# Optimization experiments

Hardware: AMD Instinct MI355X
Metric: run time of the kernel (lower is better)

## Reference

```python
import jax, jax.numpy as jnp
import numpy as np
import math

GROUPS = 32
EPS = 1e-5
NUM_HEADS = 8


def group_norm(x, gamma, beta):
    # x: [B, C, T]
    B, C, T = x.shape
    xg = x.reshape(B, GROUPS, C // GROUPS, T)
    mean = xg.mean(axis=(2, 3), keepdims=True)
    var = xg.var(axis=(2, 3), keepdims=True)
    xn = (xg - mean) * jax.lax.rsqrt(var + EPS)
    return xn.reshape(B, C, T) * gamma[None, :, None] + beta[None, :, None]


def qkv_attention(qkv, num_heads):
    # qkv: [B, 3C, T]
    B, C3, T = qkv.shape
    split = C3 // (3 * num_heads)  # head dim
    q, k, v = jnp.split(qkv, 3, axis=1)
    scale = 1.0 / math.sqrt(math.sqrt(split))
    q = (q * scale).reshape(B * num_heads, split, T)
    k = (k * scale).reshape(B * num_heads, split, T)
    v = v.reshape(B * num_heads, split, T)
    w = jnp.einsum('bct,bcs->bts', q, k)
    w = jax.nn.softmax(w.astype(jnp.float32), axis=-1).astype(w.dtype)
    out = jnp.einsum('bts,bcs->bct', w, v)
    return out.reshape(B, -1, T)


def setup_inputs() -> dict:
    key = jax.random.key(0)
    ks = jax.random.split(key, 6)
    B, C, H, W = 16, 512, 32, 32
    x = jax.random.normal(ks[0], (B, C, H, W), dtype=jnp.float32)
    gamma = jnp.ones((C,), jnp.float32)
    beta = jnp.zeros((C,), jnp.float32)
    w_qkv = jax.random.normal(ks[1], (3 * C, C), jnp.float32) * (1.0 / math.sqrt(C))
    b_qkv = jax.random.normal(ks[2], (3 * C,), jnp.float32) * 0.01
    # proj is zero-initialized in the module; use small random weights so the
    # full op chain (proj + residual) is numerically exercised.
    w_proj = jax.random.normal(ks[3], (C, C), jnp.float32) * (1.0 / math.sqrt(C))
    b_proj = jax.random.normal(ks[4], (C,), jnp.float32) * 0.01
    return {"x": x, "gamma": gamma, "beta": beta, "w_qkv": w_qkv,
            "b_qkv": b_qkv, "w_proj": w_proj, "b_proj": b_proj}


def reference(x, gamma, beta, w_qkv, b_qkv, w_proj, b_proj):
    b, c = x.shape[0], x.shape[1]
    spatial = x.shape[2:]
    xf = x.reshape(b, c, -1)                     # [B, C, T]
    xn = group_norm(xf, gamma, beta)
    qkv = jnp.einsum('oc,bct->bot', w_qkv, xn) + b_qkv[None, :, None]
    h = qkv_attention(qkv, NUM_HEADS)
    h = jnp.einsum('oc,bct->bot', w_proj, h) + b_proj[None, :, None]
    # NOTE: residual uses the normalized x (x is reassigned before norm in torch code)
    return (xn + h).reshape(b, c, *spatial)
```

## Files before the change

### kernel.cpp

```cpp
#include <hip/hip_runtime.h>

typedef __attribute__((ext_vector_type(8))) short s16x8;
typedef __attribute__((ext_vector_type(8))) unsigned short u16x8;
typedef __attribute__((ext_vector_type(4))) float f32x4;
typedef __attribute__((ext_vector_type(16))) float f32x16;

#define DEV static __device__ __forceinline__

DEV unsigned short f2bf(float f){
  union { float f; unsigned u; } v; v.f = f;
  unsigned u = v.u;
  return (unsigned short)((u + 0x7FFFu + ((u >> 16) & 1u)) >> 16);
}

DEV unsigned cvt_pk(float lo, float hi){
  unsigned r;
  asm("v_cvt_pk_bf16_f32 %0, %1, %2" : "=v"(r) : "v"(lo), "v"(hi));
  return r;
}

DEV void pl32_swap(unsigned &d, unsigned &s){
  asm("v_permlane32_swap_b32 %0, %1" : "+v"(d), "+v"(s));
}

DEV void gload16(const void* g, void* l){
  __builtin_amdgcn_global_load_lds((const __attribute__((address_space(1))) void*)g,
                                   (__attribute__((address_space(3))) void*)l, 16, 0, 0);
}

__global__ __launch_bounds__(256) void k_gncvt(const float* __restrict__ x,
    const float* __restrict__ gamma, const float* __restrict__ beta,
    float* __restrict__ stats, unsigned short* __restrict__ xt,
    const float* __restrict__ w_qkv, const float* __restrict__ w_proj,
    unsigned short* __restrict__ w_bf){
  __shared__ unsigned short lt[1024 * 16];
  __shared__ float red[8];
  __shared__ float sh_ms[2];
  const int bid = blockIdx.x;
  const int tid = threadIdx.x;

  if (bid >= 512){
    int i = (bid - 512) * 256 + tid;
    const float4* src = (i < 196608) ? (const float4*)w_qkv + i
                                     : (const float4*)w_proj + (i - 196608);
    float4 v = *src;
    unsigned long long p = (unsigned long long)f2bf(v.x)
                         | ((unsigned long long)f2bf(v.y) << 16)
                         | ((unsigned long long)f2bf(v.z) << 32)
                         | ((unsigned long long)f2bf(v.w) << 48);
    *(unsigned long long*)(w_bf + (size_t)i * 4) = p;
    return;
  }

  const int b = bid >> 5, g = bid & 31;
  const float* base = x + ((size_t)(b * 512 + g * 16)) * 1024;

  float4 vv[16];
  float s = 0.f, ss = 0.f;
  #pragma unroll
  for (int i = 0; i < 16; ++i){
    vv[i] = *(const float4*)(base + i * 1024 + tid * 4);
    s  += vv[i].x + vv[i].y + vv[i].z + vv[i].w;
    ss += vv[i].x * vv[i].x + vv[i].y * vv[i].y + vv[i].z * vv[i].z + vv[i].w * vv[i].w;
  }
  #pragma unroll
  for (int d = 1; d < 64; d <<= 1){ s += __shfl_xor(s, d); ss += __shfl_xor(ss, d); }
  if ((tid & 63) == 0){ red[tid >> 6] = s; red[4 + (tid >> 6)] = ss; }
  __syncthreads();
  if (tid == 0){
    float ts  = red[0] + red[1] + red[2] + red[3];
    float tss = red[4] + red[5] + red[6] + red[7];
    float mean = ts * (1.f / 16384.f);
    float var  = tss * (1.f / 16384.f) - mean * mean;
    float rstd = rsqrtf(var + 1e-5f);
    sh_ms[0] = mean; sh_ms[1] = rstd;
    stats[(size_t)bid * 2] = mean;
    stats[(size_t)bid * 2 + 1] = rstd;
  }
  __syncthreads();
  const float mean = sh_ms[0], rstd = sh_ms[1];

  unsigned short vals[4][16];
  #pragma unroll
  for (int i = 0; i < 16; ++i){
    float gsc = gamma[g * 16 + i] * rstd;
    float bof = beta[g * 16 + i] - mean * gsc;
    vals[0][i] = f2bf(vv[i].x * gsc + bof);
    vals[1][i] = f2bf(vv[i].y * gsc + bof);
    vals[2][i] = f2bf(vv[i].z * gsc + bof);
    vals[3][i] = f2bf(vv[i].w * gsc + bof);
  }
  #pragma unroll
  for (int k2 = 0; k2 < 4; ++k2){
    u16x8 lo, hi;
    #pragma unroll
    for (int e = 0; e < 8; ++e){ lo[e] = vals[k2][e]; hi[e] = vals[k2][8 + e]; }
    int t = tid * 4 + k2;
    *(u16x8*)&lt[t * 16]     = lo;
    *(u16x8*)&lt[t * 16 + 8] = hi;
  }
  __syncthreads();
  unsigned short* dst = xt + ((size_t)b * 1024) * 512 + g * 16;
  #pragma unroll
  for (int j = 0; j < 8; ++j){
    int idx = j * 256 + tid;
    int t = idx >> 1, half = idx & 1;
    u16x8 v = *(const u16x8*)&lt[t * 16 + half * 8];
    *(u16x8*)(dst + (size_t)t * 512 + half * 8) = v;
  }
}

DEV void gemm_mainloop(const unsigned short* __restrict__ pA,
                       const unsigned short* __restrict__ pB,
                       unsigned short* As, unsigned short* Bs,
                       f32x4 (&acc)[4][4], int tid){
  const int lane = tid & 63, wv = tid >> 6;
  const int wr = wv >> 1, wc = wv & 1;
  const int ro = lane & 15;
  for (int k0 = 0; k0 < 512; k0 += 64){
    #pragma unroll
    for (int it = 0; it < 4; ++it){
      int chunk = it * 256 + tid;
      int r = chunk >> 3, sb = chunk & 7;
      size_t goff = (size_t)r * 512 + k0 + ((sb ^ (r & 7)) << 3);
      gload16(pA + goff, As + (size_t)(it * 256 + wv * 64) * 8);
      gload16(pB + goff, Bs + (size_t)(it * 256 + wv * 64) * 8);
    }
    __syncthreads();
    #pragma unroll
    for (int kk = 0; kk < 2; ++kk){
      s16x8 a[4], bb[4];
      int ko = kk * 64 + ((lane >> 4) << 4);
      #pragma unroll
      for (int i2 = 0; i2 < 4; ++i2){
        int ra = wr * 64 + i2 * 16 + ro;
        a[i2]  = *(const s16x8*)((const char*)As + ra * 128 + (ko ^ ((ra & 7) << 4)));
        int rb = wc * 64 + i2 * 16 + ro;
        bb[i2] = *(const s16x8*)((const char*)Bs + rb * 128 + (ko ^ ((rb & 7) << 4)));
      }
      __builtin_amdgcn_s_setprio(1);
      #pragma unroll
      for (int i2 = 0; i2 < 4; ++i2)
        #pragma unroll
        for (int j2 = 0; j2 < 4; ++j2)
          acc[i2][j2] = __builtin_amdgcn_mfma_f32_16x16x32_bf16(a[i2], bb[j2], acc[i2][j2], 0, 0, 0);
      __builtin_amdgcn_s_setprio(0);
    }
    __syncthreads();
  }
}

__global__ __launch_bounds__(256) void k_qkv(const unsigned short* __restrict__ W,
    const unsigned short* __restrict__ Xt, const float* __restrict__ bias,
    unsigned short* __restrict__ qkt, unsigned short* __restrict__ vbuf){
  __shared__ unsigned short As[128 * 64], Bs[128 * 64];
  const int bid = blockIdx.x;
  const int nt = bid & 7; const int tmp = bid >> 3;
  const int mt = tmp % 12, b = tmp / 12;
  const int tid = threadIdx.x;
  const unsigned short* Wt = W + (size_t)mt * 128 * 512;
  const unsigned short* Xb = Xt + ((size_t)(b * 1024) + nt * 128) * 512;
  f32x4 acc[4][4];
  #pragma unroll
  for (int i = 0; i < 4; ++i)
    #pragma unroll
    for (int j = 0; j < 4; ++j) acc[i][j] = f32x4{0.f, 0.f, 0.f, 0.f};
  const bool isv = (mt >= 8);
  if (isv) gemm_mainloop(Wt, Xb, As, Bs, acc, tid);
  else     gemm_mainloop(Xb, Wt, As, Bs, acc, tid);
  const int lane = tid & 63, wv = tid >> 6, wr = wv >> 1, wc = wv & 1;
  const int col = lane & 15, rq = (lane >> 4) << 2;
  if (isv){
    #pragma unroll
    for (int i = 0; i < 4; ++i){
      #pragma unroll
      for (int jj = 0; jj < 4; ++jj){
        int og = mt * 128 + wr * 64 + i * 16 + rq + jj;
        float bv = bias[og];
        unsigned short* drow = vbuf + ((size_t)(b * 512) + (og - 1024)) * 1024 + nt * 128 + wc * 64;
        #pragma unroll
        for (int j = 0; j < 4; ++j)
          drow[j * 16 + col] = f2bf(acc[i][j][jj] + bv);
      }
    }
  } else {
    #pragma unroll
    for (int i = 0; i < 4; ++i){
      #pragma unroll
      for (int jj = 0; jj < 4; ++jj){
        int tg = nt * 128 + wr * 64 + i * 16 + rq + jj;
        unsigned short* drow = qkt + ((size_t)(b * 1024) + tg) * 1024 + mt * 128 + wc * 64;
        #pragma unroll
        for (int j = 0; j < 4; ++j){
          int og = mt * 128 + wc * 64 + j * 16 + col;
          drow[j * 16 + col] = f2bf(acc[i][j][jj] + bias[og]);
        }
      }
    }
  }
}

__global__ __launch_bounds__(256, 4) void k_attn(const unsigned short* __restrict__ qkt,
    const unsigned short* __restrict__ vbuf, unsigned short* __restrict__ ht){
  __shared__ __align__(16) unsigned short smem[16384];

  const int bid = blockIdx.x;
  const int xcd = bid & 7, slot = bid >> 3;
  const int qt = slot & 7;
  const int b = slot >> 3, h = xcd;
  const int tid = threadIdx.x, lane = tid & 63, wv = tid >> 6;
  const int l31 = lane & 31, hi = lane >> 5;
  const int wq0 = qt * 128 + wv * 32;
  const float CSC = 0.125f * 1.44269504f;
  const float M0 = 8.f;

  s16x8 qf[4];
  {
    const unsigned short* qrow = qkt + ((size_t)(b * 1024) + wq0 + l31) * 1024 + h * 64 + hi * 8;
    #pragma unroll
    for (int kk = 0; kk < 4; ++kk)
      qf[kk] = *(const s16x8*)(qrow + kk * 16);
  }

  f32x16 o_acc[2];
  #pragma unroll
  for (int mi = 0; mi < 2; ++mi)
    #pragma unroll
    for (int e = 0; e < 16; ++e) o_acc[mi][e] = 0.f;
  float l_run = 0.f;

  const int r0 = tid >> 3;
  const int so = ((tid & 7) ^ (r0 & 7)) << 3;
  const unsigned short* pK = qkt + (size_t)(b * 1024) * 1024 + 512 + h * 64
                           + (size_t)r0 * 1024 + so;
  const unsigned short* pV = vbuf + ((size_t)(b * 512) + h * 64) * 1024
                           + (size_t)r0 * 1024 + so;
  const size_t IT1 = (size_t)32 * 1024;

  #define STAGE(bsel) do {                                                   \
    unsigned short* Kd = smem + (bsel) * 8192;                               \
    unsigned short* Vd = Kd + 4096;                                          \
    gload16(pK,       Kd + (size_t)(wv * 64) * 8);                           \
    gload16(pK + IT1, Kd + (size_t)(256 + wv * 64) * 8);                     \
    gload16(pV,       Vd + (size_t)(wv * 64) * 8);                           \
    gload16(pV + IT1, Vd + (size_t)(256 + wv * 64) * 8);                     \
    pK += 64 * 1024; pV += 64;                                               \
  } while (0)

  STAGE(0);
  __syncthreads();
  int cur = 0;

  for (int t = 0; t < 16; ++t){
    if (t < 15) STAGE(cur ^ 1);
    const unsigned short* Ks = smem + cur * 8192;
    const unsigned short* Vs = Ks + 4096;

    f32x16 sa[2];
    #pragma unroll
    for (int ni = 0; ni < 2; ++ni)
      #pragma unroll
      for (int e = 0; e < 16; ++e) sa[ni][e] = 0.f;
    #pragma unroll
    for (int kk = 0; kk < 4; ++kk){
      s16x8 kf[2];
      #pragma unroll
      for (int ni = 0; ni < 2; ++ni){
        int r = ni * 32 + l31;
        kf[ni] = *(const s16x8*)((const char*)Ks + r * 128 + ((kk * 32 + hi * 16) ^ ((r & 7) << 4)));
      }
      __builtin_amdgcn_s_setprio(1);
      sa[0] = __builtin_amdgcn_mfma_f32_32x32x16_bf16(kf[0], qf[kk], sa[0], 0, 0, 0);
      sa[1] = __builtin_amdgcn_mfma_f32_32x32x16_bf16(kf[1], qf[kk], sa[1], 0, 0, 0);
      __builtin_amdgcn_s_setprio(0);
    }

    float rsa = 0.f, rsb = 0.f;
    unsigned pk[2][4][2];
    #pragma unroll
    for (int ni = 0; ni < 2; ++ni)
      #pragma unroll
      for (int rr = 0; rr < 4; ++rr){
        float p0 = __builtin_amdgcn_exp2f(fmaf(sa[ni][4 * rr + 0], CSC, -M0));
        float p1 = __builtin_amdgcn_exp2f(fmaf(sa[ni][4 * rr + 1], CSC, -M0));
        float p2 = __builtin_amdgcn_exp2f(fmaf(sa[ni][4 * rr + 2], CSC, -M0));
        float p3 = __builtin_amdgcn_exp2f(fmaf(sa[ni][4 * rr + 3], CSC, -M0));
        rsa += p0 + p1;
        rsb += p2 + p3;
        pk[ni][rr][0] = cvt_pk(p0, p1);
        pk[ni][rr][1] = cvt_pk(p2, p3);
      }
    {
      union { float f; unsigned u; } ua, ub;
      ua.f = rsa + rsb; ub.u = ua.u;
      pl32_swap(ua.u, ub.u);
      l_run += ua.f + ub.f;
    }

    #pragma unroll
    for (int ks = 0; ks < 4; ++ks){
      int ni = ks >> 1, q2 = (ks & 1) * 2;
      unsigned d0 = pk[ni][q2][0],     d1 = pk[ni][q2][1];
      unsigned s0 = pk[ni][q2 + 1][0], s1 = pk[ni][q2 + 1][1];
      pl32_swap(d0, s0);
      pl32_swap(d1, s1);
      union { unsigned u[4]; s16x8 v; } pb;
      pb.u[0] = d0;
      pb.u[1] = d1;
      pb.u[2] = s0;
      pb.u[3] = s1;
      s16x8 vf[2];
      #pragma unroll
      for (int mi = 0; mi < 2; ++mi){
        int c = mi * 32 + l31;
        vf[mi] = *(const s16x8*)((const char*)Vs + c * 128 + ((ks * 32 + hi * 16) ^ ((c & 7) << 4)));
      }
      __builtin_amdgcn_s_setprio(1);
      o_acc[0] = __builtin_amdgcn_mfma_f32_32x32x16_bf16(vf[0], pb.v, o_acc[0], 0, 0, 0);
      o_acc[1] = __builtin_amdgcn_mfma_f32_32x32x16_bf16(vf[1], pb.v, o_acc[1], 0, 0, 0);
      __builtin_amdgcn_s_setprio(0);
    }

    asm volatile("s_waitcnt vmcnt(0)" ::: "memory");
    __builtin_amdgcn_sched_barrier(0);
    __syncthreads();
    cur ^= 1;
  }
  #undef STAGE

  float invl = 1.f / l_run;
  unsigned short* ow = smem + wv * 2048;
  int t = l31;
  #pragma unroll
  for (int mi = 0; mi < 2; ++mi)
    #pragma unroll
    for (int rr = 0; rr < 4; ++rr){
      int c0 = mi * 32 + 8 * rr + 4 * hi;
      unsigned d0 = cvt_pk(o_acc[mi][4 * rr + 0] * invl, o_acc[mi][4 * rr + 1] * invl);
      unsigned d1 = cvt_pk(o_acc[mi][4 * rr + 2] * invl, o_acc[mi][4 * rr + 3] * invl);
      unsigned* dst = (unsigned*)(ow + t * 64 + (c0 ^ ((t & 7) << 3)));
      dst[0] = d0; dst[1] = d1;
    }
  __syncthreads();
  unsigned short* hbase = ht + ((size_t)(b * 1024) + wq0) * 512 + h * 64;
  #pragma unroll
  for (int i = 0; i < 4; ++i){
    int id = i * 64 + lane;
    int tl = id >> 3, c8 = id & 7;
    u16x8 v = *(const u16x8*)(ow + tl * 64 + ((c8 ^ (tl & 7)) << 3));
    *(u16x8*)(hbase + (size_t)tl * 512 + c8 * 8) = v;
  }
}

__global__ __launch_bounds__(256) void k_proj(const unsigned short* __restrict__ Wp,
    const unsigned short* __restrict__ Ht, const float* __restrict__ bias,
    const float* __restrict__ x, const float* __restrict__ stats,
    const float* __restrict__ gamma, const float* __restrict__ beta,
    float* __restrict__ out){
  __shared__ unsigned short As[128 * 64], Bs[128 * 64];
  const int bid = blockIdx.x;
  const int nt = bid & 7, mt = (bid >> 3) & 3, b = bid >> 5;
  const int tid = threadIdx.x;
  f32x4 acc[4][4];
  #pragma unroll
  for (int i = 0; i < 4; ++i)
    #pragma unroll
    for (int j = 0; j < 4; ++j) acc[i][j] = f32x4{0.f, 0.f, 0.f, 0.f};
  gemm_mainloop(Wp + (size_t)mt * 128 * 512,
                Ht + ((size_t)(b * 1024) + nt * 128) * 512, As, Bs, acc, tid);
  const int lane = tid & 63, wv = tid >> 6, wr = wv >> 1, wc = wv & 1;
  const int col = lane & 15, rq = (lane >> 4) << 2;
  #pragma unroll
  for (int i = 0; i < 4; ++i){
    #pragma unroll
    for (int jj = 0; jj < 4; ++jj){
      int og = mt * 128 + wr * 64 + i * 16 + rq + jj;
      float mean = stats[(size_t)(b * 32 + (og >> 4)) * 2];
      float rstd = stats[(size_t)(b * 32 + (og >> 4)) * 2 + 1];
      float gsc = gamma[og] * rstd;
      float bof = beta[og] - mean * gsc + bias[og];
      const float* xrow = x  + ((size_t)(b * 512) + og) * 1024 + nt * 128 + wc * 64;
      float* orow      = out + ((size_t)(b * 512) + og) * 1024 + nt * 128 + wc * 64;
      #pragma unroll
      for (int j = 0; j < 4; ++j){
        float xv = xrow[j * 16 + col];
        orow[j * 16 + col] = acc[i][j][jj] + xv * gsc + bof;
      }
    }
  }
}

extern "C" void kernel_launch(void* const* d_in, const int* in_sizes, int n_in,
                              void* d_out, int out_size, void* d_ws, size_t ws_size,
                              hipStream_t stream) {
  (void)in_sizes; (void)n_in; (void)out_size; (void)ws_size;
  const float* x      = (const float*)d_in[0];
  const float* gamma  = (const float*)d_in[1];
  const float* beta   = (const float*)d_in[2];
  const float* w_qkv  = (const float*)d_in[3];
  const float* b_qkv  = (const float*)d_in[4];
  const float* w_proj = (const float*)d_in[5];
  const float* b_proj = (const float*)d_in[6];
  float* out = (float*)d_out;
  char* ws = (char*)d_ws;

  unsigned short* wq_bf = (unsigned short*)ws;
  unsigned short* wp_bf = (unsigned short*)(ws + 1572864);
  float*          stats = (float*)(ws + 2097152);
  unsigned short* Xt    = (unsigned short*)(ws + 2101248);
  unsigned short* qkt   = (unsigned short*)(ws + 18878464);
  unsigned short* vbuf  = (unsigned short*)(ws + 52432896);

  k_gncvt<<<1536, 256, 0, stream>>>(x, gamma, beta, stats, Xt, w_qkv, w_proj, wq_bf);
  k_qkv<<<1536, 256, 0, stream>>>(wq_bf, Xt, b_qkv, qkt, vbuf);
  unsigned short* Ht = Xt;
  k_attn<<<1024, 256, 0, stream>>>(qkt, vbuf, Ht);
  k_proj<<<512, 256, 0, stream>>>(wp_bf, Ht, b_proj, x, stats, gamma, beta, out);
}
```

Measured before the change: 119.5 us.

## Load attention K/V fragments directly from global memory instead of LDS staging

Drops the double-buffered LDS staging of K and V tiles in the attention kernel. Each wave now loads its MFMA operand fragments straight from global memory into registers, and the per-iteration barriers and waitcnt go away. Shared memory is halved to just what the output transpose needs. In exchange, the four waves of a block each fetch the same K/V data redundantly through the cache, and global load latency is no longer hidden by explicit prefetching.

```diff
diff --git a/kernel.cpp b/kernel.cpp
--- a/kernel.cpp
+++ b/kernel.cpp
@@ -202,7 +202,7 @@
 
 __global__ __launch_bounds__(256, 4) void k_attn(const unsigned short* __restrict__ qkt,
     const unsigned short* __restrict__ vbuf, unsigned short* __restrict__ ht){
-  __shared__ __align__(16) unsigned short smem[16384];
+  __shared__ __align__(16) unsigned short smem[8192];
 
   const int bid = blockIdx.x;
   const int xcd = bid & 7, slot = bid >> 3;
@@ -229,32 +229,18 @@
     for (int e = 0; e < 16; ++e) o_acc[mi][e] = 0.f;
   float l_run = 0.f;
 
-  const int r0 = tid >> 3;
-  const int so = ((tid & 7) ^ (r0 & 7)) << 3;
-  const unsigned short* pK = qkt + (size_t)(b * 1024) * 1024 + 512 + h * 64
-                           + (size_t)r0 * 1024 + so;
-  const unsigned short* pV = vbuf + ((size_t)(b * 512) + h * 64) * 1024
-                           + (size_t)r0 * 1024 + so;
-  const size_t IT1 = (size_t)32 * 1024;
-
-  #define STAGE(bsel) do {                                                   \
-    unsigned short* Kd = smem + (bsel) * 8192;                               \
-    unsigned short* Vd = Kd + 4096;                                          \
-    gload16(pK,       Kd + (size_t)(wv * 64) * 8);                           \
-    gload16(pK + IT1, Kd + (size_t)(256 + wv * 64) * 8);                     \
-    gload16(pV,       Vd + (size_t)(wv * 64) * 8);                           \
-    gload16(pV + IT1, Vd + (size_t)(256 + wv * 64) * 8);                     \
-    pK += 64 * 1024; pV += 64;                                               \
-  } while (0)
-
-  STAGE(0);
-  __syncthreads();
-  int cur = 0;
+  const unsigned short* pK0 = qkt + ((size_t)(b * 1024) + l31) * 1024 + 512 + h * 64 + hi * 8;
+  const unsigned short* pK1 = pK0 + (size_t)32 * 1024;
+  const unsigned short* pV0 = vbuf + ((size_t)(b * 512) + h * 64 + l31) * 1024 + hi * 8;
+  const unsigned short* pV1 = pV0 + (size_t)32 * 1024;
 
   for (int t = 0; t < 16; ++t){
-    if (t < 15) STAGE(cur ^ 1);
-    const unsigned short* Ks = smem + cur * 8192;
-    const unsigned short* Vs = Ks + 4096;
+    s16x8 kf[4][2];
+    #pragma unroll
+    for (int kk = 0; kk < 4; ++kk){
+      kf[kk][0] = *(const s16x8*)(pK0 + kk * 16);
+      kf[kk][1] = *(const s16x8*)(pK1 + kk * 16);
+    }
 
     f32x16 sa[2];
     #pragma unroll
@@ -263,15 +249,9 @@
       for (int e = 0; e < 16; ++e) sa[ni][e] = 0.f;
     #pragma unroll
     for (int kk = 0; kk < 4; ++kk){
-      s16x8 kf[2];
-      #pragma unroll
-      for (int ni = 0; ni < 2; ++ni){
-        int r = ni * 32 + l31;
-        kf[ni] = *(const s16x8*)((const char*)Ks + r * 128 + ((kk * 32 + hi * 16) ^ ((r & 7) << 4)));
-      }
       __builtin_amdgcn_s_setprio(1);
-      sa[0] = __builtin_amdgcn_mfma_f32_32x32x16_bf16(kf[0], qf[kk], sa[0], 0, 0, 0);
-      sa[1] = __builtin_amdgcn_mfma_f32_32x32x16_bf16(kf[1], qf[kk], sa[1], 0, 0, 0);
+      sa[0] = __builtin_amdgcn_mfma_f32_32x32x16_bf16(kf[kk][0], qf[kk], sa[0], 0, 0, 0);
+      sa[1] = __builtin_amdgcn_mfma_f32_32x32x16_bf16(kf[kk][1], qf[kk], sa[1], 0, 0, 0);
       __builtin_amdgcn_s_setprio(0);
     }
 
@@ -309,24 +289,17 @@
       pb.u[1] = d1;
       pb.u[2] = s0;
       pb.u[3] = s1;
-      s16x8 vf[2];
-      #pragma unroll
-      for (int mi = 0; mi < 2; ++mi){
-        int c = mi * 32 + l31;
-        vf[mi] = *(const s16x8*)((const char*)Vs + c * 128 + ((ks * 32 + hi * 16) ^ ((c & 7) << 4)));
-      }
+      s16x8 vf0 = *(const s16x8*)(pV0 + ks * 16);
+      s16x8 vf1 = *(const s16x8*)(pV1 + ks * 16);
       __builtin_amdgcn_s_setprio(1);
-      o_acc[0] = __builtin_amdgcn_mfma_f32_32x32x16_bf16(vf[0], pb.v, o_acc[0], 0, 0, 0);
-      o_acc[1] = __builtin_amdgcn_mfma_f32_32x32x16_bf16(vf[1], pb.v, o_acc[1], 0, 0, 0);
+      o_acc[0] = __builtin_amdgcn_mfma_f32_32x32x16_bf16(vf0, pb.v, o_acc[0], 0, 0, 0);
+      o_acc[1] = __builtin_amdgcn_mfma_f32_32x32x16_bf16(vf1, pb.v, o_acc[1], 0, 0, 0);
       __builtin_amdgcn_s_setprio(0);
     }
 
-    asm volatile("s_waitcnt vmcnt(0)" ::: "memory");
-    __builtin_amdgcn_sched_barrier(0);
-    __syncthreads();
-    cur ^= 1;
-  }
-  #undef STAGE
+    pK0 += (size_t)64 * 1024; pK1 += (size_t)64 * 1024;
+    pV0 += 64; pV1 += 64;
+  }
 
   float invl = 1.f / l_run;
   unsigned short* ow = smem + wv * 2048;
```

Result: slower. 190.2 us (+59.2%).

## Reuse bf16 normalized activations for residual and write attention output into qkt

Applied to the files above, without the earlier changes.

The attention output is now written in place into the Q/K buffer (row stride 1024) instead of overwriting Xt, which keeps the bf16 normalized activations alive. The projection epilogue then reads the residual from that bf16 Xt tile, staged through shared memory, instead of re-reading fp32 x and recomputing the normalization from stored stats and gamma/beta. This halves residual read traffic and drops the stats buffer, at the cost of a bf16-rounded residual and a transposed LDS staging step. Overwriting qkt assumes each attention block has finished reading its Q/K rows before it writes them.

```diff
diff --git a/kernel.cpp b/kernel.cpp
--- a/kernel.cpp
+++ b/kernel.cpp
@@ -2,6 +2,7 @@
 
 typedef __attribute__((ext_vector_type(8))) short s16x8;
 typedef __attribute__((ext_vector_type(8))) unsigned short u16x8;
+typedef __attribute__((ext_vector_type(4))) unsigned short u16x4;
 typedef __attribute__((ext_vector_type(4))) float f32x4;
 typedef __attribute__((ext_vector_type(16))) float f32x16;
 
@@ -13,6 +14,11 @@
   return (unsigned short)((u + 0x7FFFu + ((u >> 16) & 1u)) >> 16);
 }
 
+DEV float bf2f(unsigned short b){
+  union { unsigned u; float f; } v; v.u = ((unsigned)b) << 16;
+  return v.f;
+}
+
 DEV unsigned cvt_pk(float lo, float hi){
   unsigned r;
   asm("v_cvt_pk_bf16_f32 %0, %1, %2" : "=v"(r) : "v"(lo), "v"(hi));
@@ -30,7 +36,7 @@
 
 __global__ __launch_bounds__(256) void k_gncvt(const float* __restrict__ x,
     const float* __restrict__ gamma, const float* __restrict__ beta,
-    float* __restrict__ stats, unsigned short* __restrict__ xt,
+    unsigned short* __restrict__ xt,
     const float* __restrict__ w_qkv, const float* __restrict__ w_proj,
     unsigned short* __restrict__ w_bf){
   __shared__ unsigned short lt[1024 * 16];
@@ -74,8 +80,6 @@
     float var  = tss * (1.f / 16384.f) - mean * mean;
     float rstd = rsqrtf(var + 1e-5f);
     sh_ms[0] = mean; sh_ms[1] = rstd;
-    stats[(size_t)bid * 2] = mean;
-    stats[(size_t)bid * 2 + 1] = rstd;
   }
   __syncthreads();
   const float mean = sh_ms[0], rstd = sh_ms[1];
@@ -113,7 +117,7 @@
 DEV void gemm_mainloop(const unsigned short* __restrict__ pA,
                        const unsigned short* __restrict__ pB,
                        unsigned short* As, unsigned short* Bs,
-                       f32x4 (&acc)[4][4], int tid){
+                       f32x4 (&acc)[4][4], int tid, int ldb){
   const int lane = tid & 63, wv = tid >> 6;
   const int wr = wv >> 1, wc = wv & 1;
   const int ro = lane & 15;
@@ -122,9 +126,9 @@
     for (int it = 0; it < 4; ++it){
       int chunk = it * 256 + tid;
       int r = chunk >> 3, sb = chunk & 7;
-      size_t goff = (size_t)r * 512 + k0 + ((sb ^ (r & 7)) << 3);
-      gload16(pA + goff, As + (size_t)(it * 256 + wv * 64) * 8);
-      gload16(pB + goff, Bs + (size_t)(it * 256 + wv * 64) * 8);
+      int soff = k0 + ((sb ^ (r & 7)) << 3);
+      gload16(pA + (size_t)r * 512 + soff, As + (size_t)(it * 256 + wv * 64) * 8);
+      gload16(pB + (size_t)r * ldb + soff, Bs + (size_t)(it * 256 + wv * 64) * 8);
     }
     __syncthreads();
     #pragma unroll
@@ -166,8 +170,8 @@
     #pragma unroll
     for (int j = 0; j < 4; ++j) acc[i][j] = f32x4{0.f, 0.f, 0.f, 0.f};
   const bool isv = (mt >= 8);
-  if (isv) gemm_mainloop(Wt, Xb, As, Bs, acc, tid);
-  else     gemm_mainloop(Xb, Wt, As, Bs, acc, tid);
+  if (isv) gemm_mainloop(Wt, Xb, As, Bs, acc, tid, 512);
+  else     gemm_mainloop(Xb, Wt, As, Bs, acc, tid, 512);
   const int lane = tid & 63, wv = tid >> 6, wr = wv >> 1, wc = wv & 1;
   const int col = lane & 15, rq = (lane >> 4) << 2;
   if (isv){
@@ -200,8 +204,8 @@
   }
 }
 
-__global__ __launch_bounds__(256, 4) void k_attn(const unsigned short* __restrict__ qkt,
-    const unsigned short* __restrict__ vbuf, unsigned short* __restrict__ ht){
+__global__ __launch_bounds__(256, 4) void k_attn(unsigned short* __restrict__ qkt,
+    const unsigned short* __restrict__ vbuf){
   __shared__ __align__(16) unsigned short smem[16384];
 
   const int bid = blockIdx.x;
@@ -342,22 +346,22 @@
       dst[0] = d0; dst[1] = d1;
     }
   __syncthreads();
-  unsigned short* hbase = ht + ((size_t)(b * 1024) + wq0) * 512 + h * 64;
+  unsigned short* hbase = qkt + ((size_t)(b * 1024) + wq0) * 1024 + h * 64;
   #pragma unroll
   for (int i = 0; i < 4; ++i){
     int id = i * 64 + lane;
     int tl = id >> 3, c8 = id & 7;
     u16x8 v = *(const u16x8*)(ow + tl * 64 + ((c8 ^ (tl & 7)) << 3));
-    *(u16x8*)(hbase + (size_t)tl * 512 + c8 * 8) = v;
+    *(u16x8*)(hbase + (size_t)tl * 1024 + c8 * 8) = v;
   }
 }
 
 __global__ __launch_bounds__(256) void k_proj(const unsigned short* __restrict__ Wp,
     const unsigned short* __restrict__ Ht, const float* __restrict__ bias,
-    const float* __restrict__ x, const float* __restrict__ stats,
-    const float* __restrict__ gamma, const float* __restrict__ beta,
-    float* __restrict__ out){
-  __shared__ unsigned short As[128 * 64], Bs[128 * 64];
+    const unsigned short* __restrict__ Xt, float* __restrict__ out){
+  __shared__ __align__(16) unsigned short smem[17408];
+  unsigned short* As = smem;
+  unsigned short* Bs = smem + 8192;
   const int bid = blockIdx.x;
   const int nt = bid & 7, mt = (bid >> 3) & 3, b = bid >> 5;
   const int tid = threadIdx.x;
@@ -367,24 +371,35 @@
     #pragma unroll
     for (int j = 0; j < 4; ++j) acc[i][j] = f32x4{0.f, 0.f, 0.f, 0.f};
   gemm_mainloop(Wp + (size_t)mt * 128 * 512,
-                Ht + ((size_t)(b * 1024) + nt * 128) * 512, As, Bs, acc, tid);
+                Ht + ((size_t)(b * 1024) + nt * 128) * 1024, As, Bs, acc, tid, 1024);
+
+  const unsigned short* xsrc = Xt + ((size_t)(b * 1024) + nt * 128) * 512 + mt * 128;
+  #pragma unroll
+  for (int p = 0; p < 8; ++p){
+    int row = p * 16 + (tid >> 4);
+    int c16 = (tid & 15) * 8;
+    *(u16x8*)(smem + row * 136 + c16) = *(const u16x8*)(xsrc + (size_t)row * 512 + c16);
+  }
+  __syncthreads();
+
   const int lane = tid & 63, wv = tid >> 6, wr = wv >> 1, wc = wv & 1;
   const int col = lane & 15, rq = (lane >> 4) << 2;
   #pragma unroll
   for (int i = 0; i < 4; ++i){
-    #pragma unroll
-    for (int jj = 0; jj < 4; ++jj){
-      int og = mt * 128 + wr * 64 + i * 16 + rq + jj;
-      float mean = stats[(size_t)(b * 32 + (og >> 4)) * 2];
-      float rstd = stats[(size_t)(b * 32 + (og >> 4)) * 2 + 1];
-      float gsc = gamma[og] * rstd;
-      float bof = beta[og] - mean * gsc + bias[og];
-      const float* xrow = x  + ((size_t)(b * 512) + og) * 1024 + nt * 128 + wc * 64;
-      float* orow      = out + ((size_t)(b * 512) + og) * 1024 + nt * 128 + wc * 64;
-      #pragma unroll
-      for (int j = 0; j < 4; ++j){
-        float xv = xrow[j * 16 + col];
-        orow[j * 16 + col] = acc[i][j][jj] + xv * gsc + bof;
+    float bv[4];
+    #pragma unroll
+    for (int jj = 0; jj < 4; ++jj)
+      bv[jj] = bias[mt * 128 + wr * 64 + i * 16 + rq + jj];
+    #pragma unroll
+    for (int j = 0; j < 4; ++j){
+      int t_l  = wc * 64 + j * 16 + col;
+      int og_l = wr * 64 + i * 16 + rq;
+      u16x4 r4 = *(const u16x4*)(smem + t_l * 136 + og_l);
+      #pragma unroll
+      for (int jj = 0; jj < 4; ++jj){
+        int og = mt * 128 + og_l + jj;
+        float* orow = out + ((size_t)(b * 512) + og) * 1024 + nt * 128 + wc * 64;
+        orow[j * 16 + col] = acc[i][j][jj] + bf2f(r4[jj]) + bv[jj];
       }
     }
   }
@@ -406,14 +421,12 @@
 
   unsigned short* wq_bf = (unsigned short*)ws;
   unsigned short* wp_bf = (unsigned short*)(ws + 1572864);
-  float*          stats = (float*)(ws + 2097152);
   unsigned short* Xt    = (unsigned short*)(ws + 2101248);
   unsigned short* qkt   = (unsigned short*)(ws + 18878464);
   unsigned short* vbuf  = (unsigned short*)(ws + 52432896);
 
-  k_gncvt<<<1536, 256, 0, stream>>>(x, gamma, beta, stats, Xt, w_qkv, w_proj, wq_bf);
+  k_gncvt<<<1536, 256, 0, stream>>>(x, gamma, beta, Xt, w_qkv, w_proj, wq_bf);
   k_qkv<<<1536, 256, 0, stream>>>(wq_bf, Xt, b_qkv, qkt, vbuf);
-  unsigned short* Ht = Xt;
-  k_attn<<<1024, 256, 0, stream>>>(qkt, vbuf, Ht);
-  k_proj<<<512, 256, 0, stream>>>(wp_bf, Ht, b_proj, x, stats, gamma, beta, out);
-}
+  k_attn<<<1024, 256, 0, stream>>>(qkt, vbuf);
+  k_proj<<<512, 256, 0, stream>>>(wp_bf, qkt, b_proj, Xt, out);
+}
```

After: 118.0 us. Within noise of the previous version (-1.2%).
